# Performance work log

Measured on AMD Instinct MI355X. Metric: run time of the kernel, lower is better.

The kernel has to match this reference:

```python
import jax, jax.numpy as jnp
import numpy as np

TOP_K = 2


def setup_inputs() -> dict:
    key = jax.random.key(0)
    ks = jax.random.split(key, 5)
    B, S, D, F, E = 2, 1024, 2048, 4096, 8
    scale_in = 1.0 / np.sqrt(D)
    scale_f = 1.0 / np.sqrt(F)
    return {
        "hidden_states": jax.random.normal(ks[0], (B, S, D), dtype=jnp.float32),
        "gate_w": jax.random.normal(ks[1], (D, E), dtype=jnp.float32) * scale_in,
        "w1": jax.random.normal(ks[2], (E, D, F), dtype=jnp.float32) * scale_in,
        "w3": jax.random.normal(ks[3], (E, D, F), dtype=jnp.float32) * scale_in,
        "w2": jax.random.normal(ks[4], (E, F, D), dtype=jnp.float32) * scale_f,
    }


def reference(hidden_states, gate_w, w1, w3, w2):
    orig_shape = hidden_states.shape
    D = orig_shape[-1]
    x = hidden_states.reshape(-1, D)                      # [T, D]
    E = gate_w.shape[-1]

    # Router: replicated linear (no bias), logits in fp32.
    router_logits = (x @ gate_w).astype(jnp.float32)      # [T, E]
    probs = jax.nn.softmax(router_logits, axis=-1)        # [T, E]
    topk_vals, topk_idx = jax.lax.top_k(probs, TOP_K)     # [T, K]
    # renormalize=False: use raw softmax probs of the selected experts.
    # Scatter top-k weights back to a dense [T, E] combine matrix.
    onehot = jax.nn.one_hot(topk_idx, E, dtype=probs.dtype)        # [T, K, E]
    combine = jnp.einsum("tke,tk->te", onehot, topk_vals)          # [T, E]

    # Dense-over-experts SwiGLU (reference for the fused grouped-GEMM).
    gate = jax.nn.silu(jnp.einsum("td,edf->etf", x, w1))  # [E, T, F]
    up = jnp.einsum("td,edf->etf", x, w3)                 # [E, T, F]
    expert_out = jnp.einsum("etf,efd->etd", gate * up, w2)  # [E, T, D]

    # Combine (this is the TP all-reduce + weighted sum in vllm).
    y = jnp.einsum("te,etd->td", combine, expert_out)     # [T, D]
    return y.reshape(orig_shape)
```

## Files before the change

kernel.cpp:

```cpp
#include <hip/hip_runtime.h>

typedef short v8s __attribute__((ext_vector_type(8)));
typedef float v4f __attribute__((ext_vector_type(4)));

#define T_TOK 2048
#define DD 2048
#define FF 4096
#define EE 8
#define BM 128
#define BN 128
#define BK 64
#define MT_MAX 40
#define MAXROWS 5120

#define WS_COUNTS 0
#define WS_FILL   32
#define WS_ROWOFF 64
#define WS_TOPE   128
#define WS_TOPW   (WS_TOPE + T_TOK * 2 * 4)
#define WS_IDS    (WS_TOPW + T_TOK * 2 * 4)
#define WS_WTS    (WS_IDS + MAXROWS * 4)
#define WS_ZERO   (WS_WTS + MAXROWS * 4)
#define WS_H      73984ul

#define SWZ(r, kb) ((((r) * 128) + (kb)) ^ (((r) & 7) << 4))

static __device__ __forceinline__ short f2bf(float f) {
  return __builtin_bit_cast(short, static_cast<__bf16>(f));
}

__global__ __launch_bounds__(256) void router_k(
    const float* __restrict__ x, const float* __restrict__ gw,
    int* __restrict__ counts, int* __restrict__ tope, float* __restrict__ topw) {
  const int lane = threadIdx.x & 63;
  const int t = blockIdx.x * 4 + (threadIdx.x >> 6);
  if (t >= T_TOK) return;
  float acc[EE] = {0.f, 0.f, 0.f, 0.f, 0.f, 0.f, 0.f, 0.f};
  const float* xr = x + (size_t)t * DD;
  for (int i = 0; i < DD / 64; ++i) {
    int k = i * 64 + lane;
    float xv = xr[k];
    const v4f* g = (const v4f*)(gw + (size_t)k * EE);
    v4f g0 = g[0], g1 = g[1];
    acc[0] += xv * g0[0]; acc[1] += xv * g0[1]; acc[2] += xv * g0[2]; acc[3] += xv * g0[3];
    acc[4] += xv * g1[0]; acc[5] += xv * g1[1]; acc[6] += xv * g1[2]; acc[7] += xv * g1[3];
  }
  #pragma unroll
  for (int e = 0; e < EE; ++e) {
    #pragma unroll
    for (int off = 32; off > 0; off >>= 1) acc[e] += __shfl_xor(acc[e], off);
  }
  if (lane == 0) {
    float m = acc[0];
    #pragma unroll
    for (int e = 1; e < EE; ++e) m = fmaxf(m, acc[e]);
    float p[EE], s = 0.f;
    #pragma unroll
    for (int e = 0; e < EE; ++e) { p[e] = expf(acc[e] - m); s += p[e]; }
    float inv = 1.f / s;
    #pragma unroll
    for (int e = 0; e < EE; ++e) p[e] *= inv;
    int e1 = 0;
    #pragma unroll
    for (int e = 1; e < EE; ++e) if (p[e] > p[e1]) e1 = e;
    int e2 = (e1 == 0) ? 1 : 0;
    #pragma unroll
    for (int e = 0; e < EE; ++e) if (e != e1 && p[e] > p[e2]) e2 = e;
    tope[2 * t] = e1;  tope[2 * t + 1] = e2;
    topw[2 * t] = p[e1]; topw[2 * t + 1] = p[e2];
    atomicAdd(&counts[e1], 1);
    atomicAdd(&counts[e2], 1);
  }
}

__global__ void offsets_k(const int* __restrict__ counts, int* __restrict__ rowoff) {
  if (threadIdx.x == 0) {
    int off = 0;
    #pragma unroll
    for (int e = 0; e < EE; ++e) {
      rowoff[e] = off;
      off += ((counts[e] + BM - 1) / BM) * BM;
    }
  }
}

__global__ __launch_bounds__(256) void scatter_k(
    const int* __restrict__ tope, const float* __restrict__ topw,
    const int* __restrict__ rowoff, int* __restrict__ fill,
    int* __restrict__ ids, float* __restrict__ wts) {
  const int t = blockIdx.x * 256 + threadIdx.x;
  if (t >= T_TOK) return;
  #pragma unroll
  for (int j = 0; j < 2; ++j) {
    int e = tope[2 * t + j];
    int pos = rowoff[e] + atomicAdd(&fill[e], 1);
    ids[pos] = t;
    wts[pos] = topw[2 * t + j];
  }
}

__global__ __launch_bounds__(256, 2) void gemm1_k(
    const float* __restrict__ x, const float* __restrict__ w1,
    const float* __restrict__ w3, const int* __restrict__ counts,
    const int* __restrict__ rowoff, const int* __restrict__ ids,
    unsigned short* __restrict__ H) {
  const int nt = blockIdx.x, mt = blockIdx.y;
  int expert = -1;
  #pragma unroll
  for (int e = 0; e < EE; ++e) {
    int rs = rowoff[e];
    int tl = (counts[e] + BM - 1) / BM;
    if (mt * BM >= rs && mt * BM < rs + tl * BM) expert = e;
  }
  if (expert < 0) return;
  const int m0 = mt * BM, n0 = nt * BN;

  __shared__ unsigned short sA[BM * BK];
  __shared__ unsigned short sB0[BN * BK];
  __shared__ unsigned short sB1[BN * BK];

  const int tid = threadIdx.x;
  const int lane = tid & 63;
  const int wid = tid >> 6;
  const int wm = (wid >> 1) * 64, wn = (wid & 1) * 64;
  const int lr = lane & 15, lg = lane >> 4;

  const int a_row0 = tid >> 3;
  const int a_kc = (tid & 7) * 8;
  const float* aptr[4];
  #pragma unroll
  for (int g = 0; g < 4; ++g)
    aptr[g] = x + (size_t)ids[m0 + a_row0 + g * 32] * DD + a_kc;

  const int b_f4 = (tid & 31) * 4;
  const int b_k8 = (tid >> 5) * 8;
  const float* wb1 = w1 + (size_t)expert * DD * FF + n0 + b_f4 + (size_t)b_k8 * FF;
  const float* wb3 = w3 + (size_t)expert * DD * FF + n0 + b_f4 + (size_t)b_k8 * FF;

  v4f acc1[4][4], acc3[4][4];
  #pragma unroll
  for (int i = 0; i < 4; ++i)
    #pragma unroll
    for (int j = 0; j < 4; ++j) {
      acc1[i][j] = (v4f){0.f, 0.f, 0.f, 0.f};
      acc3[i][j] = (v4f){0.f, 0.f, 0.f, 0.f};
    }

  for (int kt = 0; kt < DD / BK; ++kt) {
    #pragma unroll
    for (int g = 0; g < 4; ++g) {
      const float* p = aptr[g] + (size_t)kt * BK;
      v4f u0 = *(const v4f*)p;
      v4f u1 = *(const v4f*)(p + 4);
      v8s h;
      h[0] = f2bf(u0[0]); h[1] = f2bf(u0[1]); h[2] = f2bf(u0[2]); h[3] = f2bf(u0[3]);
      h[4] = f2bf(u1[0]); h[5] = f2bf(u1[1]); h[6] = f2bf(u1[2]); h[7] = f2bf(u1[3]);
      *(v8s*)((char*)sA + SWZ(a_row0 + g * 32, a_kc * 2)) = h;
    }
    {
      const float* p = wb1 + (size_t)kt * BK * FF;
      v4f r[8];
      #pragma unroll
      for (int j = 0; j < 8; ++j) r[j] = *(const v4f*)(p + (size_t)j * FF);
      #pragma unroll
      for (int c = 0; c < 4; ++c) {
        v8s h;
        #pragma unroll
        for (int j = 0; j < 8; ++j) h[j] = f2bf(r[j][c]);
        *(v8s*)((char*)sB0 + SWZ(b_f4 + c, b_k8 * 2)) = h;
      }
      p = wb3 + (size_t)kt * BK * FF;
      #pragma unroll
      for (int j = 0; j < 8; ++j) r[j] = *(const v4f*)(p + (size_t)j * FF);
      #pragma unroll
      for (int c = 0; c < 4; ++c) {
        v8s h;
        #pragma unroll
        for (int j = 0; j < 8; ++j) h[j] = f2bf(r[j][c]);
        *(v8s*)((char*)sB1 + SWZ(b_f4 + c, b_k8 * 2)) = h;
      }
    }
    __syncthreads();
    #pragma unroll
    for (int ks = 0; ks < 2; ++ks) {
      const int kb = ks * 64 + lg * 16;
      v8s a[4], b1[4], b3[4];
      #pragma unroll
      for (int m = 0; m < 4; ++m)
        a[m] = *(const v8s*)((const char*)sA + SWZ(wm + m * 16 + lr, kb));
      #pragma unroll
      for (int n = 0; n < 4; ++n) {
        b1[n] = *(const v8s*)((const char*)sB0 + SWZ(wn + n * 16 + lr, kb));
        b3[n] = *(const v8s*)((const char*)sB1 + SWZ(wn + n * 16 + lr, kb));
      }
      #pragma unroll
      for (int m = 0; m < 4; ++m)
        #pragma unroll
        for (int n = 0; n < 4; ++n) {
          acc1[m][n] = __builtin_amdgcn_mfma_f32_16x16x32_bf16(a[m], b1[n], acc1[m][n], 0, 0, 0);
          acc3[m][n] = __builtin_amdgcn_mfma_f32_16x16x32_bf16(a[m], b3[n], acc3[m][n], 0, 0, 0);
        }
    }
    __syncthreads();
  }
  #pragma unroll
  for (int m = 0; m < 4; ++m)
    #pragma unroll
    for (int n = 0; n < 4; ++n)
      #pragma unroll
      for (int r = 0; r < 4; ++r) {
        int row = wm + m * 16 + lg * 4 + r;
        int col = wn + n * 16 + lr;
        float g = acc1[m][n][r];
        float u = acc3[m][n][r];
        float hv = (g / (1.f + expf(-g))) * u;
        H[(size_t)(m0 + row) * FF + (n0 + col)] = (unsigned short)f2bf(hv);
      }
}

__global__ __launch_bounds__(256, 2) void gemm2_k(
    const unsigned short* __restrict__ H, const float* __restrict__ w2,
    const int* __restrict__ counts, const int* __restrict__ rowoff,
    const int* __restrict__ ids, const float* __restrict__ wts,
    float* __restrict__ out) {
  const int nt = blockIdx.x, mt = blockIdx.y;
  int expert = -1;
  #pragma unroll
  for (int e = 0; e < EE; ++e) {
    int rs = rowoff[e];
    int tl = (counts[e] + BM - 1) / BM;
    if (mt * BM >= rs && mt * BM < rs + tl * BM) expert = e;
  }
  if (expert < 0) return;
  const int m0 = mt * BM, n0 = nt * BN;

  __shared__ unsigned short sA[BM * BK];
  __shared__ unsigned short sB[BN * BK];

  const int tid = threadIdx.x;
  const int lane = tid & 63;
  const int wid = tid >> 6;
  const int wm = (wid >> 1) * 64, wn = (wid & 1) * 64;
  const int lr = lane & 15, lg = lane >> 4;

  const int a_row0 = tid >> 3;
  const int a_kc = (tid & 7) * 8;
  const unsigned short* ha = H + (size_t)(m0 + a_row0) * FF + a_kc;
  const int b_f4 = (tid & 31) * 4;
  const int b_k8 = (tid >> 5) * 8;
  const float* wb = w2 + (size_t)expert * FF * DD + n0 + b_f4 + (size_t)b_k8 * DD;

  v4f acc[4][4];
  #pragma unroll
  for (int i = 0; i < 4; ++i)
    #pragma unroll
    for (int j = 0; j < 4; ++j) acc[i][j] = (v4f){0.f, 0.f, 0.f, 0.f};

  for (int kt = 0; kt < FF / BK; ++kt) {
    #pragma unroll
    for (int g = 0; g < 4; ++g) {
      v8s h = *(const v8s*)(ha + (size_t)g * 32 * FF + kt * BK);
      *(v8s*)((char*)sA + SWZ(a_row0 + g * 32, a_kc * 2)) = h;
    }
    {
      const float* p = wb + (size_t)kt * BK * DD;
      v4f r[8];
      #pragma unroll
      for (int j = 0; j < 8; ++j) r[j] = *(const v4f*)(p + (size_t)j * DD);
      #pragma unroll
      for (int c = 0; c < 4; ++c) {
        v8s h;
        #pragma unroll
        for (int j = 0; j < 8; ++j) h[j] = f2bf(r[j][c]);
        *(v8s*)((char*)sB + SWZ(b_f4 + c, b_k8 * 2)) = h;
      }
    }
    __syncthreads();
    #pragma unroll
    for (int ks = 0; ks < 2; ++ks) {
      const int kb = ks * 64 + lg * 16;
      v8s a[4], b[4];
      #pragma unroll
      for (int m = 0; m < 4; ++m)
        a[m] = *(const v8s*)((const char*)sA + SWZ(wm + m * 16 + lr, kb));
      #pragma unroll
      for (int n = 0; n < 4; ++n)
        b[n] = *(const v8s*)((const char*)sB + SWZ(wn + n * 16 + lr, kb));
      #pragma unroll
      for (int m = 0; m < 4; ++m)
        #pragma unroll
        for (int n = 0; n < 4; ++n)
          acc[m][n] = __builtin_amdgcn_mfma_f32_16x16x32_bf16(a[m], b[n], acc[m][n], 0, 0, 0);
    }
    __syncthreads();
  }
  #pragma unroll
  for (int m = 0; m < 4; ++m)
    #pragma unroll
    for (int r = 0; r < 4; ++r) {
      int row = m0 + wm + m * 16 + lg * 4 + r;
      float wgt = wts[row];
      float* orow = out + (size_t)ids[row] * DD + n0 + wn + lr;
      #pragma unroll
      for (int n = 0; n < 4; ++n)
        atomicAdd(orow + n * 16, wgt * acc[m][n][r]);
    }
}

extern "C" void kernel_launch(void* const* d_in, const int* in_sizes, int n_in,
                              void* d_out, int out_size, void* d_ws, size_t ws_size,
                              hipStream_t stream) {
  const float* x  = (const float*)d_in[0];
  const float* gw = (const float*)d_in[1];
  const float* w1 = (const float*)d_in[2];
  const float* w3 = (const float*)d_in[3];
  const float* w2 = (const float*)d_in[4];
  float* out = (float*)d_out;
  char* ws = (char*)d_ws;

  int*   counts = (int*)(ws + WS_COUNTS);
  int*   fill   = (int*)(ws + WS_FILL);
  int*   rowoff = (int*)(ws + WS_ROWOFF);
  int*   tope   = (int*)(ws + WS_TOPE);
  float* topw   = (float*)(ws + WS_TOPW);
  int*   ids    = (int*)(ws + WS_IDS);
  float* wts    = (float*)(ws + WS_WTS);
  unsigned short* H = (unsigned short*)(ws + WS_H);

  hipMemsetAsync(ws, 0, WS_ZERO, stream);
  hipMemsetAsync(d_out, 0, (size_t)out_size * sizeof(float), stream);

  router_k<<<T_TOK / 4, 256, 0, stream>>>(x, gw, counts, tope, topw);
  offsets_k<<<1, 64, 0, stream>>>(counts, rowoff);
  scatter_k<<<T_TOK / 256, 256, 0, stream>>>(tope, topw, rowoff, fill, ids, wts);
  gemm1_k<<<dim3(FF / BN, MT_MAX), 256, 0, stream>>>(x, w1, w3, counts, rowoff, ids, H);
  gemm2_k<<<dim3(DD / BN, MT_MAX), 256, 0, stream>>>(H, w2, counts, rowoff, ids, wts, out);
}
```

Measured before the change: 602.5 us.

## Enlarge GEMM tiles to 256 rows with double-buffered LDS weight pipeline

Both grouped GEMMs move to 512-thread blocks with 256-row M tiles, and gemm2 also widens N to 256. Weight tiles are double-buffered in LDS, with register prefetch of the next tile issued while the current one is computed. Activations are now loaded straight from global memory into MFMA operand registers, so they no longer pass through LDS. The gemm1 SwiGLU epilogue exchanges up-projection accumulators through LDS, since different waves now hold the gate and up halves, and gemm2 skips atomics for padded rows. Larger tiles mean more padding per expert and higher register pressure, and the direct global A loads may be poorly coalesced.

```diff
diff --git a/kernel.cpp b/kernel.cpp
--- a/kernel.cpp
+++ b/kernel.cpp
@@ -7,11 +7,9 @@
 #define DD 2048
 #define FF 4096
 #define EE 8
-#define BM 128
-#define BN 128
-#define BK 64
-#define MT_MAX 40
-#define MAXROWS 5120
+#define BMG 256
+#define MT1 24
+#define MAXROWS 6144
 
 #define WS_COUNTS 0
 #define WS_FILL   32
@@ -21,9 +19,14 @@
 #define WS_IDS    (WS_TOPW + T_TOK * 2 * 4)
 #define WS_WTS    (WS_IDS + MAXROWS * 4)
 #define WS_ZERO   (WS_WTS + MAXROWS * 4)
-#define WS_H      73984ul
-
-#define SWZ(r, kb) ((((r) * 128) + (kb)) ^ (((r) & 7) << 4))
+#define WS_H      82176ul
+
+#define SWZ8(r) (((((r) ^ ((r) >> 3)) & 7)) << 4)
+#define TADDR(fl, kb) ((fl) * 128 + ((kb) ^ SWZ8(fl)))
+
+#define LGKM0() asm volatile("s_waitcnt lgkmcnt(0)" ::: "memory")
+#define BARR()  __builtin_amdgcn_s_barrier()
+#define CFENCE() asm volatile("" ::: "memory")
 
 static __device__ __forceinline__ short f2bf(float f) {
   return __builtin_bit_cast(short, static_cast<__bf16>(f));
@@ -79,7 +82,7 @@
     #pragma unroll
     for (int e = 0; e < EE; ++e) {
       rowoff[e] = off;
-      off += ((counts[e] + BM - 1) / BM) * BM;
+      off += ((counts[e] + BMG - 1) / BMG) * BMG;
     }
   }
 }
@@ -99,7 +102,7 @@
   }
 }
 
-__global__ __launch_bounds__(256, 2) void gemm1_k(
+__global__ __launch_bounds__(512, 2) void gemm1_k(
     const float* __restrict__ x, const float* __restrict__ w1,
     const float* __restrict__ w3, const int* __restrict__ counts,
     const int* __restrict__ rowoff, const int* __restrict__ ids,
@@ -109,116 +112,128 @@
   #pragma unroll
   for (int e = 0; e < EE; ++e) {
     int rs = rowoff[e];
-    int tl = (counts[e] + BM - 1) / BM;
-    if (mt * BM >= rs && mt * BM < rs + tl * BM) expert = e;
+    int tl = (counts[e] + BMG - 1) >> 8;
+    if (mt * BMG >= rs && mt * BMG < rs + tl * BMG) expert = e;
   }
   if (expert < 0) return;
-  const int m0 = mt * BM, n0 = nt * BN;
-
-  __shared__ unsigned short sA[BM * BK];
-  __shared__ unsigned short sB0[BN * BK];
-  __shared__ unsigned short sB1[BN * BK];
+  const int m0 = mt * BMG, n0 = nt * 128;
+
+  __shared__ char smem[65536];
 
   const int tid = threadIdx.x;
   const int lane = tid & 63;
   const int wid = tid >> 6;
-  const int wm = (wid >> 1) * 64, wn = (wid & 1) * 64;
   const int lr = lane & 15, lg = lane >> 4;
-
-  const int a_row0 = tid >> 3;
-  const int a_kc = (tid & 7) * 8;
-  const float* aptr[4];
-  #pragma unroll
-  for (int g = 0; g < 4; ++g)
-    aptr[g] = x + (size_t)ids[m0 + a_row0 + g * 32] * DD + a_kc;
-
-  const int b_f4 = (tid & 31) * 4;
-  const int b_k8 = (tid >> 5) * 8;
-  const float* wb1 = w1 + (size_t)expert * DD * FF + n0 + b_f4 + (size_t)b_k8 * FF;
-  const float* wb3 = w3 + (size_t)expert * DD * FF + n0 + b_f4 + (size_t)b_k8 * FF;
-
-  v4f acc1[4][4], acc3[4][4];
-  #pragma unroll
-  for (int i = 0; i < 4; ++i)
-    #pragma unroll
-    for (int j = 0; j < 4; ++j) {
-      acc1[i][j] = (v4f){0.f, 0.f, 0.f, 0.f};
-      acc3[i][j] = (v4f){0.f, 0.f, 0.f, 0.f};
-    }
-
-  for (int kt = 0; kt < DD / BK; ++kt) {
-    #pragma unroll
-    for (int g = 0; g < 4; ++g) {
-      const float* p = aptr[g] + (size_t)kt * BK;
-      v4f u0 = *(const v4f*)p;
-      v4f u1 = *(const v4f*)(p + 4);
-      v8s h;
-      h[0] = f2bf(u0[0]); h[1] = f2bf(u0[1]); h[2] = f2bf(u0[2]); h[3] = f2bf(u0[3]);
-      h[4] = f2bf(u1[0]); h[5] = f2bf(u1[1]); h[6] = f2bf(u1[2]); h[7] = f2bf(u1[3]);
-      *(v8s*)((char*)sA + SWZ(a_row0 + g * 32, a_kc * 2)) = h;
-    }
-    {
-      const float* p = wb1 + (size_t)kt * BK * FF;
-      v4f r[8];
+  const int wr = wid >> 2;
+  const int wc = wid & 3;
+  const int mat = wc >> 1;
+  const int c64 = (wc & 1) * 64;
+  const int bsub = wc * 8192;
+
+  const float* ap[8];
+  #pragma unroll
+  for (int m = 0; m < 8; ++m)
+    ap[m] = x + (size_t)ids[m0 + wr * 128 + m * 16 + lr] * DD + lg * 8;
+
+  const int smat = tid >> 8;
+  const int sr = tid & 255;
+  const int f4 = (sr & 31) * 4;
+  const int k8 = (sr >> 5) * 8;
+  const float* wsrc = (smat ? w3 : w1) + (size_t)expert * DD * FF
+                      + (size_t)k8 * FF + n0 + f4;
+
+  v4f srg[8];
+  #define G1_ISSUE(KT) { const float* sp = wsrc + (size_t)(KT) * 64 * FF;       \
+    _Pragma("unroll") for (int j = 0; j < 8; ++j)                               \
+      srg[j] = *(const v4f*)(sp + (size_t)j * FF); }
+  #define G1_WRITE(BUF) { _Pragma("unroll") for (int c = 0; c < 4; ++c) {       \
+      v8s h; _Pragma("unroll") for (int j = 0; j < 8; ++j) h[j] = f2bf(srg[j][c]); \
+      int fg = f4 + c;                                                          \
+      *(v8s*)(smem + (BUF) * 32768 + (smat * 2 + (fg >> 6)) * 8192              \
+              + TADDR((fg & 63), k8 * 2)) = h; } }
+
+  v4f acc[8][4];
+  #pragma unroll
+  for (int i = 0; i < 8; ++i)
+    #pragma unroll
+    for (int j = 0; j < 4; ++j) acc[i][j] = (v4f){0.f, 0.f, 0.f, 0.f};
+
+  G1_ISSUE(0);
+  G1_WRITE(0);
+  G1_ISSUE(1);
+  LGKM0(); BARR(); CFENCE();
+
+  const int NKT = DD / 64;
+  #pragma unroll 2
+  for (int kt = 0; kt < NKT; ++kt) {
+    const int cur = kt & 1;
+    #pragma unroll
+    for (int ks = 0; ks < 2; ++ks) {
+      v8s b0 = *(const v8s*)(smem + cur * 32768 + bsub + TADDR(0 * 16 + lr, ks * 64 + lg * 16));
+      v8s b1 = *(const v8s*)(smem + cur * 32768 + bsub + TADDR(1 * 16 + lr, ks * 64 + lg * 16));
+      v8s b2 = *(const v8s*)(smem + cur * 32768 + bsub + TADDR(2 * 16 + lr, ks * 64 + lg * 16));
+      v8s b3 = *(const v8s*)(smem + cur * 32768 + bsub + TADDR(3 * 16 + lr, ks * 64 + lg * 16));
       #pragma unroll
-      for (int j = 0; j < 8; ++j) r[j] = *(const v4f*)(p + (size_t)j * FF);
+      for (int m = 0; m < 8; ++m) {
+        const float* p = ap[m] + kt * 64 + ks * 32;
+        v4f u0 = *(const v4f*)p;
+        v4f u1 = *(const v4f*)(p + 4);
+        v8s av;
+        av[0] = f2bf(u0[0]); av[1] = f2bf(u0[1]); av[2] = f2bf(u0[2]); av[3] = f2bf(u0[3]);
+        av[4] = f2bf(u1[0]); av[5] = f2bf(u1[1]); av[6] = f2bf(u1[2]); av[7] = f2bf(u1[3]);
+        acc[m][0] = __builtin_amdgcn_mfma_f32_16x16x32_bf16(av, b0, acc[m][0], 0, 0, 0);
+        acc[m][1] = __builtin_amdgcn_mfma_f32_16x16x32_bf16(av, b1, acc[m][1], 0, 0, 0);
+        acc[m][2] = __builtin_amdgcn_mfma_f32_16x16x32_bf16(av, b2, acc[m][2], 0, 0, 0);
+        acc[m][3] = __builtin_amdgcn_mfma_f32_16x16x32_bf16(av, b3, acc[m][3], 0, 0, 0);
+      }
+    }
+    LGKM0(); CFENCE(); BARR(); CFENCE();
+    if (kt + 1 < NKT) {
+      G1_WRITE(1 - cur);
+      if (kt + 2 < NKT) G1_ISSUE(kt + 2);
+      LGKM0();
+    }
+    CFENCE(); BARR(); CFENCE();
+  }
+
+  const int ebase = (wr * 2 + (wc & 1)) * 16384;
+  #pragma unroll
+  for (int pass = 0; pass < 2; ++pass) {
+    if (mat == 1) {
       #pragma unroll
-      for (int c = 0; c < 4; ++c) {
-        v8s h;
-        #pragma unroll
-        for (int j = 0; j < 8; ++j) h[j] = f2bf(r[j][c]);
-        *(v8s*)((char*)sB0 + SWZ(b_f4 + c, b_k8 * 2)) = h;
-      }
-      p = wb3 + (size_t)kt * BK * FF;
-      #pragma unroll
-      for (int j = 0; j < 8; ++j) r[j] = *(const v4f*)(p + (size_t)j * FF);
-      #pragma unroll
-      for (int c = 0; c < 4; ++c) {
-        v8s h;
-        #pragma unroll
-        for (int j = 0; j < 8; ++j) h[j] = f2bf(r[j][c]);
-        *(v8s*)((char*)sB1 + SWZ(b_f4 + c, b_k8 * 2)) = h;
-      }
-    }
-    __syncthreads();
-    #pragma unroll
-    for (int ks = 0; ks < 2; ++ks) {
-      const int kb = ks * 64 + lg * 16;
-      v8s a[4], b1[4], b3[4];
-      #pragma unroll
-      for (int m = 0; m < 4; ++m)
-        a[m] = *(const v8s*)((const char*)sA + SWZ(wm + m * 16 + lr, kb));
-      #pragma unroll
-      for (int n = 0; n < 4; ++n) {
-        b1[n] = *(const v8s*)((const char*)sB0 + SWZ(wn + n * 16 + lr, kb));
-        b3[n] = *(const v8s*)((const char*)sB1 + SWZ(wn + n * 16 + lr, kb));
-      }
-      #pragma unroll
-      for (int m = 0; m < 4; ++m)
+      for (int mm = 0; mm < 4; ++mm) {
         #pragma unroll
         for (int n = 0; n < 4; ++n) {
-          acc1[m][n] = __builtin_amdgcn_mfma_f32_16x16x32_bf16(a[m], b1[n], acc1[m][n], 0, 0, 0);
-          acc3[m][n] = __builtin_amdgcn_mfma_f32_16x16x32_bf16(a[m], b3[n], acc3[m][n], 0, 0, 0);
+          int col = n * 16 + lr;
+          *(v4f*)(smem + ebase + col * 256 + ((mm * 64 + lg * 16) ^ SWZ8(col))) =
+              acc[pass * 4 + mm][n];
         }
-    }
-    __syncthreads();
-  }
-  #pragma unroll
-  for (int m = 0; m < 4; ++m)
-    #pragma unroll
-    for (int n = 0; n < 4; ++n)
+      }
+    }
+    LGKM0(); CFENCE(); BARR(); CFENCE();
+    if (mat == 0) {
       #pragma unroll
-      for (int r = 0; r < 4; ++r) {
-        int row = wm + m * 16 + lg * 4 + r;
-        int col = wn + n * 16 + lr;
-        float g = acc1[m][n][r];
-        float u = acc3[m][n][r];
-        float hv = (g / (1.f + expf(-g))) * u;
-        H[(size_t)(m0 + row) * FF + (n0 + col)] = (unsigned short)f2bf(hv);
-      }
-}
-
-__global__ __launch_bounds__(256, 2) void gemm2_k(
+      for (int mm = 0; mm < 4; ++mm) {
+        int m = pass * 4 + mm;
+        #pragma unroll
+        for (int n = 0; n < 4; ++n) {
+          int col = n * 16 + lr;
+          v4f up = *(const v4f*)(smem + ebase + col * 256 + ((mm * 64 + lg * 16) ^ SWZ8(col)));
+          #pragma unroll
+          for (int r = 0; r < 4; ++r) {
+            float g = acc[m][n][r];
+            float hv = (g / (1.f + expf(-g))) * up[r];
+            H[(size_t)(m0 + wr * 128 + m * 16 + lg * 4 + r) * FF
+              + (n0 + c64 + n * 16 + lr)] = (unsigned short)f2bf(hv);
+          }
+        }
+      }
+    }
+    CFENCE(); BARR(); CFENCE();
+  }
+}
+
+__global__ __launch_bounds__(512, 2) void gemm2_k(
     const unsigned short* __restrict__ H, const float* __restrict__ w2,
     const int* __restrict__ counts, const int* __restrict__ rowoff,
     const int* __restrict__ ids, const float* __restrict__ wts,
@@ -228,83 +243,100 @@
   #pragma unroll
   for (int e = 0; e < EE; ++e) {
     int rs = rowoff[e];
-    int tl = (counts[e] + BM - 1) / BM;
-    if (mt * BM >= rs && mt * BM < rs + tl * BM) expert = e;
+    int tl = (counts[e] + BMG - 1) >> 8;
+    if (mt * BMG >= rs && mt * BMG < rs + tl * BMG) expert = e;
   }
   if (expert < 0) return;
-  const int m0 = mt * BM, n0 = nt * BN;
-
-  __shared__ unsigned short sA[BM * BK];
-  __shared__ unsigned short sB[BN * BK];
+  const int m0 = mt * BMG, n0 = nt * 256;
+
+  __shared__ char smem[65536];
 
   const int tid = threadIdx.x;
   const int lane = tid & 63;
   const int wid = tid >> 6;
-  const int wm = (wid >> 1) * 64, wn = (wid & 1) * 64;
   const int lr = lane & 15, lg = lane >> 4;
-
-  const int a_row0 = tid >> 3;
-  const int a_kc = (tid & 7) * 8;
-  const unsigned short* ha = H + (size_t)(m0 + a_row0) * FF + a_kc;
-  const int b_f4 = (tid & 31) * 4;
-  const int b_k8 = (tid >> 5) * 8;
-  const float* wb = w2 + (size_t)expert * FF * DD + n0 + b_f4 + (size_t)b_k8 * DD;
-
-  v4f acc[4][4];
-  #pragma unroll
-  for (int i = 0; i < 4; ++i)
+  const int wr = wid >> 2;
+  const int wq = wid & 3;
+  const int bsub = wq * 8192;
+
+  const unsigned short* hp[8];
+  #pragma unroll
+  for (int m = 0; m < 8; ++m)
+    hp[m] = H + (size_t)(m0 + wr * 128 + m * 16 + lr) * FF + lg * 8;
+
+  const int d4 = (tid & 63) * 4;
+  const int k8 = (tid >> 6) * 8;
+  const float* wsrc = w2 + (size_t)expert * FF * DD + (size_t)k8 * DD + n0 + d4;
+
+  v4f srg[8];
+  #define G2_ISSUE(KT) { const float* sp = wsrc + (size_t)(KT) * 64 * DD;       \
+    _Pragma("unroll") for (int j = 0; j < 8; ++j)                               \
+      srg[j] = *(const v4f*)(sp + (size_t)j * DD); }
+  #define G2_WRITE(BUF) { _Pragma("unroll") for (int c = 0; c < 4; ++c) {       \
+      v8s h; _Pragma("unroll") for (int j = 0; j < 8; ++j) h[j] = f2bf(srg[j][c]); \
+      int dg = d4 + c;                                                          \
+      *(v8s*)(smem + (BUF) * 32768 + (dg >> 6) * 8192                           \
+              + TADDR((dg & 63), k8 * 2)) = h; } }
+
+  v4f acc[8][4];
+  #pragma unroll
+  for (int i = 0; i < 8; ++i)
     #pragma unroll
     for (int j = 0; j < 4; ++j) acc[i][j] = (v4f){0.f, 0.f, 0.f, 0.f};
 
-  for (int kt = 0; kt < FF / BK; ++kt) {
-    #pragma unroll
-    for (int g = 0; g < 4; ++g) {
-      v8s h = *(const v8s*)(ha + (size_t)g * 32 * FF + kt * BK);
-      *(v8s*)((char*)sA + SWZ(a_row0 + g * 32, a_kc * 2)) = h;
-    }
-    {
-      const float* p = wb + (size_t)kt * BK * DD;
-      v4f r[8];
+  v8s apre[8];
+  #define G2_APRE(KT) { _Pragma("unroll") for (int m = 0; m < 8; ++m)           \
+      apre[m] = *(const v8s*)(hp[m] + (KT) * 64); }
+
+  G2_ISSUE(0);
+  G2_WRITE(0);
+  G2_ISSUE(1);
+  G2_APRE(0);
+  LGKM0(); BARR(); CFENCE();
+
+  const int NKT = FF / 64;
+  #pragma unroll 2
+  for (int kt = 0; kt < NKT; ++kt) {
+    const int cur = kt & 1;
+    #pragma unroll
+    for (int ks = 0; ks < 2; ++ks) {
+      v8s b0 = *(const v8s*)(smem + cur * 32768 + bsub + TADDR(0 * 16 + lr, ks * 64 + lg * 16));
+      v8s b1 = *(const v8s*)(smem + cur * 32768 + bsub + TADDR(1 * 16 + lr, ks * 64 + lg * 16));
+      v8s b2 = *(const v8s*)(smem + cur * 32768 + bsub + TADDR(2 * 16 + lr, ks * 64 + lg * 16));
+      v8s b3 = *(const v8s*)(smem + cur * 32768 + bsub + TADDR(3 * 16 + lr, ks * 64 + lg * 16));
       #pragma unroll
-      for (int j = 0; j < 8; ++j) r[j] = *(const v4f*)(p + (size_t)j * DD);
-      #pragma unroll
-      for (int c = 0; c < 4; ++c) {
-        v8s h;
-        #pragma unroll
-        for (int j = 0; j < 8; ++j) h[j] = f2bf(r[j][c]);
-        *(v8s*)((char*)sB + SWZ(b_f4 + c, b_k8 * 2)) = h;
-      }
-    }
-    __syncthreads();
-    #pragma unroll
-    for (int ks = 0; ks < 2; ++ks) {
-      const int kb = ks * 64 + lg * 16;
-      v8s a[4], b[4];
-      #pragma unroll
-      for (int m = 0; m < 4; ++m)
-        a[m] = *(const v8s*)((const char*)sA + SWZ(wm + m * 16 + lr, kb));
-      #pragma unroll
-      for (int n = 0; n < 4; ++n)
-        b[n] = *(const v8s*)((const char*)sB + SWZ(wn + n * 16 + lr, kb));
-      #pragma unroll
-      for (int m = 0; m < 4; ++m)
+      for (int m = 0; m < 8; ++m) {
+        v8s av = ks ? *(const v8s*)(hp[m] + kt * 64 + 32) : apre[m];
+        acc[m][0] = __builtin_amdgcn_mfma_f32_16x16x32_bf16(av, b0, acc[m][0], 0, 0, 0);
+        acc[m][1] = __builtin_amdgcn_mfma_f32_16x16x32_bf16(av, b1, acc[m][1], 0, 0, 0);
+        acc[m][2] = __builtin_amdgcn_mfma_f32_16x16x32_bf16(av, b2, acc[m][2], 0, 0, 0);
+        acc[m][3] = __builtin_amdgcn_mfma_f32_16x16x32_bf16(av, b3, acc[m][3], 0, 0, 0);
+      }
+    }
+    LGKM0(); CFENCE(); BARR(); CFENCE();
+    if (kt + 1 < NKT) {
+      G2_WRITE(1 - cur);
+      if (kt + 2 < NKT) G2_ISSUE(kt + 2);
+      G2_APRE(kt + 1);
+      LGKM0();
+    }
+    CFENCE(); BARR(); CFENCE();
+  }
+
+  #pragma unroll
+  for (int m = 0; m < 8; ++m) {
+    #pragma unroll
+    for (int r = 0; r < 4; ++r) {
+      int row = m0 + wr * 128 + m * 16 + lg * 4 + r;
+      float wgt = wts[row];
+      if (wgt != 0.f) {
+        float* orow = out + (size_t)ids[row] * DD + n0 + wq * 64 + lr;
         #pragma unroll
         for (int n = 0; n < 4; ++n)
-          acc[m][n] = __builtin_amdgcn_mfma_f32_16x16x32_bf16(a[m], b[n], acc[m][n], 0, 0, 0);
-    }
-    __syncthreads();
-  }
-  #pragma unroll
-  for (int m = 0; m < 4; ++m)
-    #pragma unroll
-    for (int r = 0; r < 4; ++r) {
-      int row = m0 + wm + m * 16 + lg * 4 + r;
-      float wgt = wts[row];
-      float* orow = out + (size_t)ids[row] * DD + n0 + wn + lr;
-      #pragma unroll
-      for (int n = 0; n < 4; ++n)
-        atomicAdd(orow + n * 16, wgt * acc[m][n][r]);
-    }
+          atomicAdd(orow + n * 16, wgt * acc[m][n][r]);
+      }
+    }
+  }
 }
 
 extern "C" void kernel_launch(void* const* d_in, const int* in_sizes, int n_in,
@@ -333,6 +365,6 @@
   router_k<<<T_TOK / 4, 256, 0, stream>>>(x, gw, counts, tope, topw);
   offsets_k<<<1, 64, 0, stream>>>(counts, rowoff);
   scatter_k<<<T_TOK / 256, 256, 0, stream>>>(tope, topw, rowoff, fill, ids, wts);
-  gemm1_k<<<dim3(FF / BN, MT_MAX), 256, 0, stream>>>(x, w1, w3, counts, rowoff, ids, H);
-  gemm2_k<<<dim3(DD / BN, MT_MAX), 256, 0, stream>>>(H, w2, counts, rowoff, ids, wts, out);
-}
+  gemm1_k<<<dim3(FF / 128, MT1), 512, 0, stream>>>(x, w1, w3, counts, rowoff, ids, H);
+  gemm2_k<<<dim3(DD / 256, MT1), 512, 0, stream>>>(H, w2, counts, rowoff, ids, wts, out);
+}
```

New measurement: 1.420 ms. 136% more time.
